# Performance work log

Hardware: AMD Instinct MI355X
Metric: run time of the kernel (lower is better)

Reference implementation:

```python
import jax, jax.numpy as jnp
import numpy as np

T, B, H = 2048, 16, 1024


def setup_inputs() -> dict:
    key = jax.random.key(0)
    k1, k2, k3 = jax.random.split(key, 3)
    inputs = jax.random.normal(k1, (T, B, H), dtype=jnp.float32)
    # torch params initialized uniform_(-0.1, 0.1)
    weight_W = jax.random.uniform(k2, (H, H), dtype=jnp.float32, minval=-0.1, maxval=0.1)
    weight_proj = jax.random.uniform(k3, (H, 1), dtype=jnp.float32, minval=-0.1, maxval=0.1)
    return {"inputs": inputs, "weight_W": weight_W, "weight_proj": weight_proj,
            "attention_width": 3}


def reference(inputs, weight_W, weight_proj, attention_width):
    # inputs: [T, B, H] (time-major). For t < w the input passes through unchanged.
    # For t >= w: attend over the previous w steps (t-w .. t-1, excluding t):
    #   score_j = tanh(h_j @ W) @ proj, a = softmax over window, out = sum_j a_j * h_j
    w = attention_width
    t = inputs.shape[0]
    n = t - w  # number of attended output positions
    # per-position scores, computed once for all timesteps: [T, B]
    scores = jnp.squeeze(jnp.tanh(inputs @ weight_W) @ weight_proj, axis=-1)
    # sliding windows via w shifted views (w is small and static)
    s_win = jnp.stack([scores[j:j + n] for j in range(w)], axis=0)   # [w, n, B]
    v_win = jnp.stack([inputs[j:j + n] for j in range(w)], axis=0)   # [w, n, B, H]
    attn = jax.nn.softmax(s_win, axis=0)                             # softmax over window
    tail = jnp.einsum('wnb,wnbh->nbh', attn, v_win)                  # [n, B, H]
    return jnp.concatenate([inputs[:w], tail], axis=0)               # [T, B, H]
```

## Files before the change

### kernel.cpp

```cpp
#include <hip/hip_runtime.h>
#include <stdint.h>

#define T_DIM 2048
#define B_DIM 16
#define H_DIM 1024
#define M_DIM (T_DIM * B_DIM)
#define BK 64
#define TCHUNK 8

typedef __attribute__((ext_vector_type(8))) short bf16x8;
typedef __attribute__((ext_vector_type(4))) float floatx4;

__device__ inline unsigned short f2bf(float f) {
  union { float f; unsigned int u; } c; c.f = f;
  unsigned int u = c.u;
  return (unsigned short)((u + 0x7FFFu + ((u >> 16) & 1u)) >> 16);
}

__device__ inline float fast_tanh(float x) {
  float e = __expf(2.0f * x);
  return 1.0f - 2.0f / (e + 1.0f);
}

__global__ void convert_x_kernel(const float* __restrict__ x,
                                 unsigned short* __restrict__ xb) {
  size_t i = ((size_t)blockIdx.x * 256 + threadIdx.x) * 4;
  float4 v = *(const float4*)(x + i);
  ushort4 o;
  o.x = f2bf(v.x); o.y = f2bf(v.y); o.z = f2bf(v.z); o.w = f2bf(v.w);
  *(ushort4*)(xb + i) = o;
}

__global__ void transpose_w_kernel(const float* __restrict__ w,
                                   unsigned short* __restrict__ wt) {
  __shared__ float tile[32][33];
  int tx = threadIdx.x, ty = threadIdx.y;
  int n0 = blockIdx.x * 32, k0 = blockIdx.y * 32;
  for (int i = ty; i < 32; i += 8)
    tile[i][tx] = w[(size_t)(k0 + i) * H_DIM + n0 + tx];
  __syncthreads();
  for (int i = ty; i < 32; i += 8)
    wt[(size_t)(n0 + i) * H_DIM + k0 + tx] = f2bf(tile[tx][i]);
}

__global__ __launch_bounds__(256, 4)
void score_gemm_kernel(const unsigned short* __restrict__ Xb,
                       const unsigned short* __restrict__ Wt,
                       const float* __restrict__ proj,
                       float* __restrict__ scores) {
  __shared__ __align__(16) unsigned short ldsA[128 * BK];
  __shared__ __align__(16) unsigned short ldsB[128 * BK];

  const int tid  = threadIdx.x;
  const int lane = tid & 63;
  const int wave = tid >> 6;
  const int wy = wave >> 1, wx = wave & 1;
  const int quad = lane >> 4, l16 = lane & 15;

  const int idx   = blockIdx.x;
  const int x7    = idx & 7;
  const int split = (idx >> 3) & 3;
  const int g     = idx >> 5;
  const int bm    = g * 8 + x7;
  const int m0    = bm * 128;
  const int nbase = split * 256;

  int ldsOff[4];
  int rowOff[4];
  #pragma unroll
  for (int i = 0; i < 4; ++i) {
    int cb = (i * 4 + wave) * 64;
    int s = cb + lane;
    int row = s >> 3, cs = s & 7;
    int cg = cs ^ (row & 7);
    ldsOff[i] = cb;
    rowOff[i] = row * H_DIM + cg * 8;
  }

  float sc[4][4];
  #pragma unroll
  for (int a = 0; a < 4; ++a)
    #pragma unroll
    for (int b = 0; b < 4; ++b) sc[a][b] = 0.0f;

  for (int n0 = nbase; n0 < nbase + 256; n0 += 128) {
    floatx4 acc[4][4];
    #pragma unroll
    for (int a = 0; a < 4; ++a)
      #pragma unroll
      for (int b = 0; b < 4; ++b) acc[a][b] = (floatx4){0.f, 0.f, 0.f, 0.f};

    for (int k0 = 0; k0 < H_DIM; k0 += BK) {
      #pragma unroll
      for (int i = 0; i < 4; ++i) {
        const unsigned short* ga = Xb + (size_t)m0 * H_DIM + rowOff[i] + k0;
        __builtin_amdgcn_global_load_lds(
            (const __attribute__((address_space(1))) void*)ga,
            (__attribute__((address_space(3))) void*)(&ldsA[ldsOff[i] * 8]),
            16, 0, 0);
        const unsigned short* gb = Wt + (size_t)n0 * H_DIM + rowOff[i] + k0;
        __builtin_amdgcn_global_load_lds(
            (const __attribute__((address_space(1))) void*)gb,
            (__attribute__((address_space(3))) void*)(&ldsB[ldsOff[i] * 8]),
            16, 0, 0);
      }
      __syncthreads();

      #pragma unroll
      for (int kk = 0; kk < BK; kk += 32) {
        const int c = (kk >> 3) + quad;
        bf16x8 af[4], bfr[4];
        #pragma unroll
        for (int rs = 0; rs < 4; ++rs) {
          int r = wy * 64 + rs * 16 + l16;
          af[rs] = *(const bf16x8*)&ldsA[(r * 8 + (c ^ (r & 7))) * 8];
        }
        #pragma unroll
        for (int ns = 0; ns < 4; ++ns) {
          int n = wx * 64 + ns * 16 + l16;
          bfr[ns] = *(const bf16x8*)&ldsB[(n * 8 + (c ^ (n & 7))) * 8];
        }
        #pragma unroll
        for (int rs = 0; rs < 4; ++rs)
          #pragma unroll
          for (int ns = 0; ns < 4; ++ns)
            acc[rs][ns] = __builtin_amdgcn_mfma_f32_16x16x32_bf16(
                af[rs], bfr[ns], acc[rs][ns], 0, 0, 0);
      }
      __syncthreads();
    }

    #pragma unroll
    for (int ns = 0; ns < 4; ++ns) {
      int n = n0 + wx * 64 + ns * 16 + l16;
      float p = proj[n];
      #pragma unroll
      for (int rs = 0; rs < 4; ++rs)
        #pragma unroll
        for (int gg = 0; gg < 4; ++gg)
          sc[rs][gg] += fast_tanh(acc[rs][ns][gg]) * p;
    }
  }

  #pragma unroll
  for (int rs = 0; rs < 4; ++rs)
    #pragma unroll
    for (int gg = 0; gg < 4; ++gg) {
      float v = sc[rs][gg];
      v += __shfl_xor(v, 1);
      v += __shfl_xor(v, 2);
      v += __shfl_xor(v, 4);
      v += __shfl_xor(v, 8);
      if (l16 == 0) {
        int row = m0 + wy * 64 + rs * 16 + quad * 4 + gg;
        atomicAdd(&scores[row], v);
      }
    }
}

__global__ void out_kernel(const float* __restrict__ x,
                           const float* __restrict__ scores,
                           const int* __restrict__ wp,
                           float* __restrict__ out) {
  int w = *wp;
  int t0 = blockIdx.x * TCHUNK;
  int b  = blockIdx.y;
  int h  = threadIdx.x;
  const float4* x4 = (const float4*)x;
  float4* o4 = (float4*)out;

  if (w == 3) {
    float4 z = {0.f, 0.f, 0.f, 0.f};
    float4 a0, a1, a2;
    float  s0, s1, s2;
    {
      int tm = t0 - 3;
      a0 = (tm >= 0) ? x4[((size_t)tm * B_DIM + b) * 256 + h] : z;
      s0 = (tm >= 0) ? scores[tm * B_DIM + b] : 0.f;
      tm = t0 - 2;
      a1 = (tm >= 0) ? x4[((size_t)tm * B_DIM + b) * 256 + h] : z;
      s1 = (tm >= 0) ? scores[tm * B_DIM + b] : 0.f;
      tm = t0 - 1;
      a2 = (tm >= 0) ? x4[((size_t)tm * B_DIM + b) * 256 + h] : z;
      s2 = (tm >= 0) ? scores[tm * B_DIM + b] : 0.f;
    }
    #pragma unroll
    for (int i = 0; i < TCHUNK; ++i) {
      int t = t0 + i;
      size_t rbase = ((size_t)t * B_DIM + b) * 256 + h;
      float4 v = x4[rbase];
      float  sv = scores[t * B_DIM + b];
      if (t < 3) {
        o4[rbase] = v;
      } else {
        float m = fmaxf(fmaxf(s0, s1), s2);
        float e0 = __expf(s0 - m), e1 = __expf(s1 - m), e2 = __expf(s2 - m);
        float inv = 1.0f / (e0 + e1 + e2);
        e0 *= inv; e1 *= inv; e2 *= inv;
        float4 o;
        o.x = e0 * a0.x + e1 * a1.x + e2 * a2.x;
        o.y = e0 * a0.y + e1 * a1.y + e2 * a2.y;
        o.z = e0 * a0.z + e1 * a1.z + e2 * a2.z;
        o.w = e0 * a0.w + e1 * a1.w + e2 * a2.w;
        o4[rbase] = o;
      }
      a0 = a1; a1 = a2; a2 = v;
      s0 = s1; s1 = s2; s2 = sv;
    }
  } else {
    if (w > 8) w = 8;
    for (int i = 0; i < TCHUNK; ++i) {
      int t = t0 + i;
      size_t rbase = ((size_t)t * B_DIM + b) * 256 + h;
      if (t < w) { o4[rbase] = x4[rbase]; continue; }
      float s[8];
      float mx = -1e30f;
      for (int j = 0; j < w; ++j) {
        s[j] = scores[(t - w + j) * B_DIM + b];
        mx = fmaxf(mx, s[j]);
      }
      float sum = 0.f;
      for (int j = 0; j < w; ++j) { s[j] = __expf(s[j] - mx); sum += s[j]; }
      float inv = 1.0f / sum;
      float4 o = {0.f, 0.f, 0.f, 0.f};
      for (int j = 0; j < w; ++j) {
        float a = s[j] * inv;
        float4 v = x4[((size_t)(t - w + j) * B_DIM + b) * 256 + h];
        o.x += a * v.x; o.y += a * v.y; o.z += a * v.z; o.w += a * v.w;
      }
      o4[rbase] = o;
    }
  }
}

extern "C" void kernel_launch(void* const* d_in, const int* in_sizes, int n_in,
                              void* d_out, int out_size, void* d_ws, size_t ws_size,
                              hipStream_t stream) {
  const float* x    = (const float*)d_in[0];
  const float* w    = (const float*)d_in[1];
  const float* proj = (const float*)d_in[2];
  const int*   wp   = (const int*)d_in[3];
  float* out = (float*)d_out;

  unsigned short* Xb = (unsigned short*)d_out;
  unsigned short* Wt = (unsigned short*)((char*)d_out + (size_t)64 * 1024 * 1024);
  float* scores = (float*)d_ws;

  hipMemsetAsync(scores, 0, M_DIM * sizeof(float), stream);

  convert_x_kernel<<<M_DIM * H_DIM / 1024, 256, 0, stream>>>(x, Xb);
  transpose_w_kernel<<<dim3(32, 32), dim3(32, 8), 0, stream>>>(w, Wt);
  score_gemm_kernel<<<1024, 256, 0, stream>>>(Xb, Wt, proj, scores);
  out_kernel<<<dim3(T_DIM / TCHUNK, B_DIM), 256, 0, stream>>>(x, scores, wp, out);
}
```

Before: 353.2 us.

## Read bf16 copy of inputs in output kernel when workspace is large enough

```diff
diff --git a/kernel.cpp b/kernel.cpp
--- a/kernel.cpp
+++ b/kernel.cpp
@@ -6,7 +6,7 @@
 #define H_DIM 1024
 #define M_DIM (T_DIM * B_DIM)
 #define BK 64
-#define TCHUNK 8
+#define TCHUNK 32
 
 typedef __attribute__((ext_vector_type(8))) short bf16x8;
 typedef __attribute__((ext_vector_type(4))) float floatx4;
@@ -15,6 +15,11 @@
   union { float f; unsigned int u; } c; c.f = f;
   unsigned int u = c.u;
   return (unsigned short)((u + 0x7FFFu + ((u >> 16) & 1u)) >> 16);
+}
+
+__device__ inline float bf2f(unsigned short u) {
+  union { float f; unsigned int u; } c; c.u = ((unsigned int)u) << 16;
+  return c.f;
 }
 
 __device__ inline float fast_tanh(float x) {
@@ -158,10 +163,90 @@
     }
 }
 
-__global__ void out_kernel(const float* __restrict__ x,
-                           const float* __restrict__ scores,
-                           const int* __restrict__ wp,
-                           float* __restrict__ out) {
+__global__ void out_kernel_bf16(const float* __restrict__ x,
+                                const unsigned short* __restrict__ xb,
+                                const float* __restrict__ scores,
+                                const int* __restrict__ wp,
+                                float* __restrict__ out) {
+  int w = *wp;
+  int t0 = blockIdx.x * TCHUNK;
+  int b  = blockIdx.y;
+  int h  = threadIdx.x;
+  const float4* x4 = (const float4*)x;
+  float4* o4 = (float4*)out;
+  const ushort4* xb4 = (const ushort4*)xb;
+
+  if (w == 3) {
+    float4 z = {0.f, 0.f, 0.f, 0.f};
+    float4 a0, a1, a2;
+    float  s0, s1, s2;
+    #pragma unroll
+    for (int j = 0; j < 3; ++j) {
+      int tm = t0 - 3 + j;
+      float4 a = z; float s = 0.f;
+      if (tm >= 0) {
+        ushort4 u = xb4[((size_t)tm * B_DIM + b) * 256 + h];
+        a.x = bf2f(u.x); a.y = bf2f(u.y); a.z = bf2f(u.z); a.w = bf2f(u.w);
+        s = scores[tm * B_DIM + b];
+      }
+      if (j == 0) { a0 = a; s0 = s; }
+      else if (j == 1) { a1 = a; s1 = s; }
+      else { a2 = a; s2 = s; }
+    }
+    for (int i = 0; i < TCHUNK; ++i) {
+      int t = t0 + i;
+      size_t rbase = ((size_t)t * B_DIM + b) * 256 + h;
+      ushort4 u = xb4[rbase];
+      float4 v;
+      v.x = bf2f(u.x); v.y = bf2f(u.y); v.z = bf2f(u.z); v.w = bf2f(u.w);
+      float sv = scores[t * B_DIM + b];
+      if (t < 3) {
+        o4[rbase] = x4[rbase];
+      } else {
+        float m = fmaxf(fmaxf(s0, s1), s2);
+        float e0 = __expf(s0 - m), e1 = __expf(s1 - m), e2 = __expf(s2 - m);
+        float inv = 1.0f / (e0 + e1 + e2);
+        e0 *= inv; e1 *= inv; e2 *= inv;
+        float4 o;
+        o.x = e0 * a0.x + e1 * a1.x + e2 * a2.x;
+        o.y = e0 * a0.y + e1 * a1.y + e2 * a2.y;
+        o.z = e0 * a0.z + e1 * a1.z + e2 * a2.z;
+        o.w = e0 * a0.w + e1 * a1.w + e2 * a2.w;
+        o4[rbase] = o;
+      }
+      a0 = a1; a1 = a2; a2 = v;
+      s0 = s1; s1 = s2; s2 = sv;
+    }
+  } else {
+    if (w > 8) w = 8;
+    for (int i = 0; i < TCHUNK; ++i) {
+      int t = t0 + i;
+      size_t rbase = ((size_t)t * B_DIM + b) * 256 + h;
+      if (t < w) { o4[rbase] = x4[rbase]; continue; }
+      float s[8];
+      float mx = -1e30f;
+      for (int j = 0; j < w; ++j) {
+        s[j] = scores[(t - w + j) * B_DIM + b];
+        mx = fmaxf(mx, s[j]);
+      }
+      float sum = 0.f;
+      for (int j = 0; j < w; ++j) { s[j] = __expf(s[j] - mx); sum += s[j]; }
+      float inv = 1.0f / sum;
+      float4 o = {0.f, 0.f, 0.f, 0.f};
+      for (int j = 0; j < w; ++j) {
+        float a = s[j] * inv;
+        float4 v = x4[((size_t)(t - w + j) * B_DIM + b) * 256 + h];
+        o.x += a * v.x; o.y += a * v.y; o.z += a * v.z; o.w += a * v.w;
+      }
+      o4[rbase] = o;
+    }
+  }
+}
+
+__global__ void out_kernel_f32(const float* __restrict__ x,
+                               const float* __restrict__ scores,
+                               const int* __restrict__ wp,
+                               float* __restrict__ out) {
   int w = *wp;
   int t0 = blockIdx.x * TCHUNK;
   int b  = blockIdx.y;
@@ -184,7 +269,6 @@
       a2 = (tm >= 0) ? x4[((size_t)tm * B_DIM + b) * 256 + h] : z;
       s2 = (tm >= 0) ? scores[tm * B_DIM + b] : 0.f;
     }
-    #pragma unroll
     for (int i = 0; i < TCHUNK; ++i) {
       int t = t0 + i;
       size_t rbase = ((size_t)t * B_DIM + b) * 256 + h;
@@ -242,14 +326,31 @@
   const int*   wp   = (const int*)d_in[3];
   float* out = (float*)d_out;
 
-  unsigned short* Xb = (unsigned short*)d_out;
-  unsigned short* Wt = (unsigned short*)((char*)d_out + (size_t)64 * 1024 * 1024);
-  float* scores = (float*)d_ws;
+  const size_t XB_BYTES = (size_t)64 * 1024 * 1024;
+  const size_t WT_BYTES = (size_t)2 * 1024 * 1024;
+  const size_t need = XB_BYTES + WT_BYTES + (size_t)M_DIM * sizeof(float);
+  const bool use_ws = ws_size >= need;
+
+  unsigned short* Xb;
+  unsigned short* Wt;
+  float* scores;
+  if (use_ws) {
+    Xb = (unsigned short*)d_ws;
+    Wt = (unsigned short*)((char*)d_ws + XB_BYTES);
+    scores = (float*)((char*)d_ws + XB_BYTES + WT_BYTES);
+  } else {
+    Xb = (unsigned short*)d_out;
+    Wt = (unsigned short*)((char*)d_out + XB_BYTES);
+    scores = (float*)d_ws;
+  }
 
   hipMemsetAsync(scores, 0, M_DIM * sizeof(float), stream);
 
   convert_x_kernel<<<M_DIM * H_DIM / 1024, 256, 0, stream>>>(x, Xb);
   transpose_w_kernel<<<dim3(32, 32), dim3(32, 8), 0, stream>>>(w, Wt);
   score_gemm_kernel<<<1024, 256, 0, stream>>>(Xb, Wt, proj, scores);
-  out_kernel<<<dim3(T_DIM / TCHUNK, B_DIM), 256, 0, stream>>>(x, scores, wp, out);
-}
+  if (use_ws)
+    out_kernel_bf16<<<dim3(T_DIM / TCHUNK, B_DIM), 256, 0, stream>>>(x, Xb, scores, wp, out);
+  else
+    out_kernel_f32<<<dim3(T_DIM / TCHUNK, B_DIM), 256, 0, stream>>>(x, scores, wp, out);
+}
```

New measurement: 333.1 us. -5.7%, faster.

## Fuse prep kernels, drop atomics, read bf16 inputs in output stage

Applied to the files above, without the earlier changes.

```diff
diff --git a/kernel.cpp b/kernel.cpp
--- a/kernel.cpp
+++ b/kernel.cpp
@@ -6,7 +6,9 @@
 #define H_DIM 1024
 #define M_DIM (T_DIM * B_DIM)
 #define BK 64
-#define TCHUNK 8
+#define TCHUNK 16
+#define CONV_BLOCKS 4096
+#define CONV_PER_THREAD 4
 
 typedef __attribute__((ext_vector_type(8))) short bf16x8;
 typedef __attribute__((ext_vector_type(4))) float floatx4;
@@ -17,37 +19,63 @@
   return (unsigned short)((u + 0x7FFFu + ((u >> 16) & 1u)) >> 16);
 }
 
+__device__ inline float bf2f(unsigned int u16) {
+  union { float f; unsigned int u; } c; c.u = u16 << 16;
+  return c.f;
+}
+
 __device__ inline float fast_tanh(float x) {
   float e = __expf(2.0f * x);
   return 1.0f - 2.0f / (e + 1.0f);
 }
 
-__global__ void convert_x_kernel(const float* __restrict__ x,
-                                 unsigned short* __restrict__ xb) {
-  size_t i = ((size_t)blockIdx.x * 256 + threadIdx.x) * 4;
-  float4 v = *(const float4*)(x + i);
-  ushort4 o;
-  o.x = f2bf(v.x); o.y = f2bf(v.y); o.z = f2bf(v.z); o.w = f2bf(v.w);
-  *(ushort4*)(xb + i) = o;
-}
-
-__global__ void transpose_w_kernel(const float* __restrict__ w,
-                                   unsigned short* __restrict__ wt) {
+__device__ inline void unpack8(uint4 u, float* a) {
+  a[0] = bf2f(u.x & 0xffffu); a[1] = bf2f(u.x >> 16);
+  a[2] = bf2f(u.y & 0xffffu); a[3] = bf2f(u.y >> 16);
+  a[4] = bf2f(u.z & 0xffffu); a[5] = bf2f(u.z >> 16);
+  a[6] = bf2f(u.w & 0xffffu); a[7] = bf2f(u.w >> 16);
+}
+
+__global__ void prep_kernel(const float* __restrict__ x,
+                            uint4* __restrict__ xb16,
+                            const float* __restrict__ w,
+                            unsigned short* __restrict__ wt) {
   __shared__ float tile[32][33];
-  int tx = threadIdx.x, ty = threadIdx.y;
-  int n0 = blockIdx.x * 32, k0 = blockIdx.y * 32;
-  for (int i = ty; i < 32; i += 8)
-    tile[i][tx] = w[(size_t)(k0 + i) * H_DIM + n0 + tx];
-  __syncthreads();
-  for (int i = ty; i < 32; i += 8)
-    wt[(size_t)(n0 + i) * H_DIM + k0 + tx] = f2bf(tile[tx][i]);
+  const int bid = blockIdx.x;
+  const int tid = threadIdx.x;
+  if (bid < CONV_BLOCKS) {
+    const float4* x4 = (const float4*)x;
+    const size_t stride = (size_t)CONV_BLOCKS * 256;
+    size_t t0 = (size_t)bid * 256 + tid;
+    #pragma unroll
+    for (int it = 0; it < CONV_PER_THREAD; ++it) {
+      size_t o = t0 + (size_t)it * stride;
+      float4 lo = x4[o * 2];
+      float4 hi = x4[o * 2 + 1];
+      uint4 u;
+      u.x = ((unsigned)f2bf(lo.y) << 16) | f2bf(lo.x);
+      u.y = ((unsigned)f2bf(lo.w) << 16) | f2bf(lo.z);
+      u.z = ((unsigned)f2bf(hi.y) << 16) | f2bf(hi.x);
+      u.w = ((unsigned)f2bf(hi.w) << 16) | f2bf(hi.z);
+      xb16[o] = u;
+    }
+  } else {
+    const int tb = bid - CONV_BLOCKS;
+    const int tx = tid & 31, ty = tid >> 5;
+    const int n0 = (tb & 31) * 32, k0 = (tb >> 5) * 32;
+    for (int i = ty; i < 32; i += 8)
+      tile[i][tx] = w[(size_t)(k0 + i) * H_DIM + n0 + tx];
+    __syncthreads();
+    for (int i = ty; i < 32; i += 8)
+      wt[(size_t)(n0 + i) * H_DIM + k0 + tx] = f2bf(tile[tx][i]);
+  }
 }
 
 __global__ __launch_bounds__(256, 4)
 void score_gemm_kernel(const unsigned short* __restrict__ Xb,
                        const unsigned short* __restrict__ Wt,
                        const float* __restrict__ proj,
-                       float* __restrict__ scores) {
+                       float* __restrict__ scoresP) {
   __shared__ __align__(16) unsigned short ldsA[128 * BK];
   __shared__ __align__(16) unsigned short ldsB[128 * BK];
 
@@ -153,15 +181,129 @@
       v += __shfl_xor(v, 8);
       if (l16 == 0) {
         int row = m0 + wy * 64 + rs * 16 + quad * 4 + gg;
-        atomicAdd(&scores[row], v);
-      }
-    }
-}
-
-__global__ void out_kernel(const float* __restrict__ x,
-                           const float* __restrict__ scores,
-                           const int* __restrict__ wp,
-                           float* __restrict__ out) {
+        scoresP[(size_t)(split * 2 + wx) * M_DIM + row] = v;
+      }
+    }
+}
+
+__global__ void out_kernel_bf16(const float* __restrict__ x,
+                                const uint4* __restrict__ xb16,
+                                const float* __restrict__ scoresP,
+                                const int* __restrict__ wp,
+                                float* __restrict__ out) {
+  __shared__ float lds_s[2][TCHUNK + 3];
+  int w = *wp;
+  const int t0 = blockIdx.x * TCHUNK;
+  const int half = threadIdx.x >> 7;
+  const int h8 = threadIdx.x & 127;
+  const int b = blockIdx.y * 2 + half;
+  const float4* x4 = (const float4*)x;
+  float4* o4 = (float4*)out;
+
+  {
+    int nsum = 2 * (TCHUNK + 3);
+    for (int q = threadIdx.x; q < nsum; q += 256) {
+      int bs = q / (TCHUNK + 3);
+      int ti = q - bs * (TCHUNK + 3);
+      int tm = t0 - 3 + ti;
+      float s = 0.f;
+      if (tm >= 0) {
+        int bb = blockIdx.y * 2 + bs;
+        #pragma unroll
+        for (int p = 0; p < 8; ++p)
+          s += scoresP[(size_t)p * M_DIM + tm * B_DIM + bb];
+      }
+      lds_s[bs][ti] = s;
+    }
+    __syncthreads();
+  }
+
+  if (w == 3) {
+    float a[3][8];
+    float s[3];
+    #pragma unroll
+    for (int j = 0; j < 3; ++j) {
+      int tm = t0 - 3 + j;
+      s[j] = lds_s[half][j];
+      #pragma unroll
+      for (int e = 0; e < 8; ++e) a[j][e] = 0.f;
+      if (tm >= 0) {
+        uint4 u = xb16[((size_t)tm * B_DIM + b) * 128 + h8];
+        unpack8(u, a[j]);
+      }
+    }
+    #pragma unroll
+    for (int i = 0; i < TCHUNK; ++i) {
+      const int t = t0 + i;
+      const size_t rowbase = (size_t)t * B_DIM + b;
+      uint4 u = xb16[rowbase * 128 + h8];
+      float v[8];
+      unpack8(u, v);
+      float sv = lds_s[half][i + 3];
+      const int c0 = i % 3, c1 = (i + 1) % 3, c2 = (i + 2) % 3;
+      const size_t rb = rowbase * 256 + h8 * 2;
+      if (t < 3) {
+        o4[rb] = x4[rb];
+        o4[rb + 1] = x4[rb + 1];
+      } else {
+        float s0 = s[c0], s1 = s[c1], s2 = s[c2];
+        float m = fmaxf(fmaxf(s0, s1), s2);
+        float e0 = __expf(s0 - m), e1 = __expf(s1 - m), e2 = __expf(s2 - m);
+        float inv = 1.0f / (e0 + e1 + e2);
+        e0 *= inv; e1 *= inv; e2 *= inv;
+        float4 oA, oB;
+        oA.x = e0 * a[c0][0] + e1 * a[c1][0] + e2 * a[c2][0];
+        oA.y = e0 * a[c0][1] + e1 * a[c1][1] + e2 * a[c2][1];
+        oA.z = e0 * a[c0][2] + e1 * a[c1][2] + e2 * a[c2][2];
+        oA.w = e0 * a[c0][3] + e1 * a[c1][3] + e2 * a[c2][3];
+        oB.x = e0 * a[c0][4] + e1 * a[c1][4] + e2 * a[c2][4];
+        oB.y = e0 * a[c0][5] + e1 * a[c1][5] + e2 * a[c2][5];
+        oB.z = e0 * a[c0][6] + e1 * a[c1][6] + e2 * a[c2][6];
+        oB.w = e0 * a[c0][7] + e1 * a[c1][7] + e2 * a[c2][7];
+        o4[rb] = oA;
+        o4[rb + 1] = oB;
+      }
+      #pragma unroll
+      for (int e = 0; e < 8; ++e) a[c0][e] = v[e];
+      s[c0] = sv;
+    }
+  } else {
+    if (w > 8) w = 8;
+    for (int i = 0; i < TCHUNK; ++i) {
+      int t = t0 + i;
+      size_t rb = ((size_t)t * B_DIM + b) * 256 + h8 * 2;
+      if (t < w) { o4[rb] = x4[rb]; o4[rb + 1] = x4[rb + 1]; continue; }
+      float sw[8];
+      float mx = -1e30f;
+      for (int j = 0; j < w; ++j) {
+        float s = 0.f;
+        #pragma unroll
+        for (int p = 0; p < 8; ++p)
+          s += scoresP[(size_t)p * M_DIM + (t - w + j) * B_DIM + b];
+        sw[j] = s;
+        mx = fmaxf(mx, s);
+      }
+      float sum = 0.f;
+      for (int j = 0; j < w; ++j) { sw[j] = __expf(sw[j] - mx); sum += sw[j]; }
+      float inv = 1.0f / sum;
+      float4 oA = {0.f, 0.f, 0.f, 0.f}, oB = {0.f, 0.f, 0.f, 0.f};
+      for (int j = 0; j < w; ++j) {
+        float aw = sw[j] * inv;
+        size_t tb = ((size_t)(t - w + j) * B_DIM + b) * 256 + h8 * 2;
+        float4 vA = x4[tb], vB = x4[tb + 1];
+        oA.x += aw * vA.x; oA.y += aw * vA.y; oA.z += aw * vA.z; oA.w += aw * vA.w;
+        oB.x += aw * vB.x; oB.y += aw * vB.y; oB.z += aw * vB.z; oB.w += aw * vB.w;
+      }
+      o4[rb] = oA;
+      o4[rb + 1] = oB;
+    }
+  }
+}
+
+__global__ void out_kernel_f32(const float* __restrict__ x,
+                               const float* __restrict__ scoresP,
+                               const int* __restrict__ wp,
+                               float* __restrict__ out) {
   int w = *wp;
   int t0 = blockIdx.x * TCHUNK;
   int b  = blockIdx.y;
@@ -169,67 +311,31 @@
   const float4* x4 = (const float4*)x;
   float4* o4 = (float4*)out;
 
-  if (w == 3) {
-    float4 z = {0.f, 0.f, 0.f, 0.f};
-    float4 a0, a1, a2;
-    float  s0, s1, s2;
-    {
-      int tm = t0 - 3;
-      a0 = (tm >= 0) ? x4[((size_t)tm * B_DIM + b) * 256 + h] : z;
-      s0 = (tm >= 0) ? scores[tm * B_DIM + b] : 0.f;
-      tm = t0 - 2;
-      a1 = (tm >= 0) ? x4[((size_t)tm * B_DIM + b) * 256 + h] : z;
-      s1 = (tm >= 0) ? scores[tm * B_DIM + b] : 0.f;
-      tm = t0 - 1;
-      a2 = (tm >= 0) ? x4[((size_t)tm * B_DIM + b) * 256 + h] : z;
-      s2 = (tm >= 0) ? scores[tm * B_DIM + b] : 0.f;
-    }
-    #pragma unroll
-    for (int i = 0; i < TCHUNK; ++i) {
-      int t = t0 + i;
-      size_t rbase = ((size_t)t * B_DIM + b) * 256 + h;
-      float4 v = x4[rbase];
-      float  sv = scores[t * B_DIM + b];
-      if (t < 3) {
-        o4[rbase] = v;
-      } else {
-        float m = fmaxf(fmaxf(s0, s1), s2);
-        float e0 = __expf(s0 - m), e1 = __expf(s1 - m), e2 = __expf(s2 - m);
-        float inv = 1.0f / (e0 + e1 + e2);
-        e0 *= inv; e1 *= inv; e2 *= inv;
-        float4 o;
-        o.x = e0 * a0.x + e1 * a1.x + e2 * a2.x;
-        o.y = e0 * a0.y + e1 * a1.y + e2 * a2.y;
-        o.z = e0 * a0.z + e1 * a1.z + e2 * a2.z;
-        o.w = e0 * a0.w + e1 * a1.w + e2 * a2.w;
-        o4[rbase] = o;
-      }
-      a0 = a1; a1 = a2; a2 = v;
-      s0 = s1; s1 = s2; s2 = sv;
-    }
-  } else {
-    if (w > 8) w = 8;
-    for (int i = 0; i < TCHUNK; ++i) {
-      int t = t0 + i;
-      size_t rbase = ((size_t)t * B_DIM + b) * 256 + h;
-      if (t < w) { o4[rbase] = x4[rbase]; continue; }
-      float s[8];
-      float mx = -1e30f;
-      for (int j = 0; j < w; ++j) {
-        s[j] = scores[(t - w + j) * B_DIM + b];
-        mx = fmaxf(mx, s[j]);
-      }
-      float sum = 0.f;
-      for (int j = 0; j < w; ++j) { s[j] = __expf(s[j] - mx); sum += s[j]; }
-      float inv = 1.0f / sum;
-      float4 o = {0.f, 0.f, 0.f, 0.f};
-      for (int j = 0; j < w; ++j) {
-        float a = s[j] * inv;
-        float4 v = x4[((size_t)(t - w + j) * B_DIM + b) * 256 + h];
-        o.x += a * v.x; o.y += a * v.y; o.z += a * v.z; o.w += a * v.w;
-      }
-      o4[rbase] = o;
-    }
+  if (w > 8) w = 8;
+  for (int i = 0; i < TCHUNK; ++i) {
+    int t = t0 + i;
+    size_t rbase = ((size_t)t * B_DIM + b) * 256 + h;
+    if (t < w) { o4[rbase] = x4[rbase]; continue; }
+    float s[8];
+    float mx = -1e30f;
+    for (int j = 0; j < w; ++j) {
+      float sv = 0.f;
+      #pragma unroll
+      for (int p = 0; p < 8; ++p)
+        sv += scoresP[(size_t)p * M_DIM + (t - w + j) * B_DIM + b];
+      s[j] = sv;
+      mx = fmaxf(mx, sv);
+    }
+    float sum = 0.f;
+    for (int j = 0; j < w; ++j) { s[j] = __expf(s[j] - mx); sum += s[j]; }
+    float inv = 1.0f / sum;
+    float4 o = {0.f, 0.f, 0.f, 0.f};
+    for (int j = 0; j < w; ++j) {
+      float a = s[j] * inv;
+      float4 v = x4[((size_t)(t - w + j) * B_DIM + b) * 256 + h];
+      o.x += a * v.x; o.y += a * v.y; o.z += a * v.z; o.w += a * v.w;
+    }
+    o4[rbase] = o;
   }
 }
 
@@ -242,14 +348,31 @@
   const int*   wp   = (const int*)d_in[3];
   float* out = (float*)d_out;
 
-  unsigned short* Xb = (unsigned short*)d_out;
-  unsigned short* Wt = (unsigned short*)((char*)d_out + (size_t)64 * 1024 * 1024);
-  float* scores = (float*)d_ws;
-
-  hipMemsetAsync(scores, 0, M_DIM * sizeof(float), stream);
-
-  convert_x_kernel<<<M_DIM * H_DIM / 1024, 256, 0, stream>>>(x, Xb);
-  transpose_w_kernel<<<dim3(32, 32), dim3(32, 8), 0, stream>>>(w, Wt);
-  score_gemm_kernel<<<1024, 256, 0, stream>>>(Xb, Wt, proj, scores);
-  out_kernel<<<dim3(T_DIM / TCHUNK, B_DIM), 256, 0, stream>>>(x, scores, wp, out);
-}
+  const size_t XB_BYTES = (size_t)64 * 1024 * 1024;
+  const size_t WT_BYTES = (size_t)2 * 1024 * 1024;
+  const size_t SP_BYTES = (size_t)8 * M_DIM * sizeof(float);
+  const size_t need = XB_BYTES + WT_BYTES + SP_BYTES;
+  const bool use_ws = ws_size >= need;
+
+  unsigned short* Xb;
+  unsigned short* Wt;
+  float* scoresP;
+  if (use_ws) {
+    Xb = (unsigned short*)d_ws;
+    Wt = (unsigned short*)((char*)d_ws + XB_BYTES);
+    scoresP = (float*)((char*)d_ws + XB_BYTES + WT_BYTES);
+  } else {
+    Xb = (unsigned short*)d_out;
+    Wt = (unsigned short*)((char*)d_out + XB_BYTES);
+    scoresP = (float*)d_ws;
+  }
+
+  prep_kernel<<<CONV_BLOCKS + 1024, 256, 0, stream>>>(x, (uint4*)Xb, w, Wt);
+  score_gemm_kernel<<<1024, 256, 0, stream>>>(Xb, Wt, proj, scoresP);
+  if (use_ws)
+    out_kernel_bf16<<<dim3(T_DIM / TCHUNK, B_DIM / 2), 256, 0, stream>>>(
+        x, (const uint4*)Xb, scoresP, wp, out);
+  else
+    out_kernel_f32<<<dim3(T_DIM / TCHUNK, B_DIM), 256, 0, stream>>>(
+        x, scoresP, wp, out);
+}
```

After: 340.1 us. -3.7%, faster.
